# Kernel optimization log

Hardware: AMD Instinct MI355X
Metric: run time of the kernel (lower is better)

Reference implementation:

```python
import jax, jax.numpy as jnp
import numpy as np

B, S, DM = 1, 2048, 1024
H, D, T = 16, 64, 16
NA = 3  # anchor tiles per query (local tile appended -> 4 tiles, 64 tokens)


def setup_inputs() -> dict:
    key = jax.random.key(0)
    ks = jax.random.split(key, 6)
    sc = 1.0 / np.sqrt(DM)
    x = jax.random.normal(ks[0], (B, S, DM), jnp.float32)
    Wq = jax.random.normal(ks[1], (DM, H * D), jnp.float32) * sc
    Wk = jax.random.normal(ks[2], (DM, H * D), jnp.float32) * sc
    Wv = jax.random.normal(ks[3], (DM, H * D), jnp.float32) * sc
    Wo = jax.random.normal(ks[4], (H * D, DM), jnp.float32) * sc
    anchor_indices = jax.random.randint(ks[5], (B, H, S, NA), 0, S // T).astype(jnp.int32)
    # RoPE freqs: freqs_cis[s, j] = exp(i * s * theta_j), half-split convention
    half = D // 2
    inv_freq = 1.0 / (10000.0 ** (np.arange(half, dtype=np.float64) / half))
    ang = np.outer(np.arange(S), inv_freq)  # [S, half]
    cos = jnp.asarray(np.cos(ang), jnp.float32)
    sin = jnp.asarray(np.sin(ang), jnp.float32)
    return {"x": x, "Wq": Wq, "Wk": Wk, "Wv": Wv, "Wo": Wo,
            "cos": cos, "sin": sin, "anchor_indices": anchor_indices}


def _rotate_half(z):
    h = z.shape[-1] // 2
    return jnp.concatenate([-z[..., h:], z[..., :h]], axis=-1)


def reference(x, Wq, Wk, Wv, Wo, cos, sin, anchor_indices):
    b, s, _ = x.shape
    # projections -> [B, H, S, D]
    q = (x @ Wq).reshape(b, s, H, D).transpose(0, 2, 1, 3)
    k = (x @ Wk).reshape(b, s, H, D).transpose(0, 2, 1, 3)
    v = (x @ Wv).reshape(b, s, H, D).transpose(0, 2, 1, 3)
    # RoPE (half-split / rotate_half)
    cos_f = jnp.concatenate([cos, cos], axis=-1)[None, None]  # [1,1,S,D]
    sin_f = jnp.concatenate([sin, sin], axis=-1)[None, None]
    q = q * cos_f + _rotate_half(q) * sin_f
    k = k * cos_f + _rotate_half(k) * sin_f
    # tile index set: anchor tiles + local tile
    local = (jnp.arange(s) // T).astype(jnp.int32)
    local = jnp.broadcast_to(local[None, None, :, None], (b, H, s, 1))
    tiles = jnp.concatenate([anchor_indices, local], axis=-1)  # [B,H,S,NA+1]
    tok = tiles[..., None] * T + jnp.arange(T, dtype=jnp.int32)  # [B,H,S,NA+1,T]
    K = (NA + 1) * T  # sparse_len
    idx = jnp.clip(tok.reshape(b, H, s, K), 0, s - 1)
    # per-(b,h) per-query gather of K/V -> [B,H,S,K,D]
    gather = jax.vmap(jax.vmap(lambda kv, i: kv[i]))
    k_sp = gather(k, idx)
    v_sp = gather(v, idx)
    logits = jnp.einsum('bhqd,bhqkd->bhqk', q, k_sp) / jnp.sqrt(jnp.float32(D))
    qidx = jnp.arange(s)[None, None, :, None]
    fut = idx > qidx  # causal mask over gathered keys
    logits = jnp.where(fut, -1e10, logits)
    w = jax.nn.softmax(logits, axis=-1)
    fully_masked = jnp.all(fut, axis=-1, keepdims=True)
    w = jnp.where(fully_masked, 0.0, w)
    w = jnp.where(jnp.isnan(w), 0.0, w)
    out = jnp.einsum('bhqk,bhqkd->bhqd', w, v_sp)
    out = out.transpose(0, 2, 1, 3).reshape(b, s, H * D)
    return out @ Wo
```

## Files before the change

### kernel.cpp

```cpp
#include <hip/hip_runtime.h>
#include <hip/hip_bf16.h>


#define S_LEN 2048
#define DM 1024
#define NH 16
#define HD 64

typedef __bf16 bf16x8 __attribute__((ext_vector_type(8)));
typedef float f32x4 __attribute__((ext_vector_type(4)));

static __device__ __forceinline__ unsigned short f2bf(float f) {
    union { float f; unsigned int i; } un;
    un.f = f;
    unsigned int r = un.i + 0x7FFFu + ((un.i >> 16) & 1u);
    return (unsigned short)(r >> 16);
}
static __device__ __forceinline__ float bfu2f(unsigned short u) {
    union { unsigned int i; float f; } un;
    un.i = ((unsigned int)u) << 16;
    return un.f;
}
static __device__ __forceinline__ float bflo(unsigned int u) {
    union { unsigned int i; float f; } un;
    un.i = u << 16;
    return un.f;
}
static __device__ __forceinline__ float bfhi(unsigned int u) {
    union { unsigned int i; float f; } un;
    un.i = u & 0xFFFF0000u;
    return un.f;
}

static __device__ __forceinline__ void gll16(const unsigned short* g,
                                             unsigned short* l) {
    __builtin_amdgcn_global_load_lds(
        (const __attribute__((address_space(1))) unsigned int*)(uintptr_t)g,
        (__attribute__((address_space(3))) unsigned int*)(uintptr_t)l,
        16, 0, 0);
}

__global__ __launch_bounds__(256) void prep(
    const float* __restrict__ x, unsigned short* __restrict__ xb,
    const float* __restrict__ W0, const float* __restrict__ W1,
    const float* __restrict__ W2, const float* __restrict__ W3,
    unsigned short* __restrict__ T0, unsigned short* __restrict__ T1,
    unsigned short* __restrict__ T2, unsigned short* __restrict__ T3) {
    const int bx = blockIdx.x;
    if (bx < 4096) {
        const int z = bx >> 10, rem = bx & 1023;
        const float* W = (z == 0) ? W0 : (z == 1) ? W1 : (z == 2) ? W2 : W3;
        unsigned short* T = (z == 0) ? T0 : (z == 1) ? T1 : (z == 2) ? T2 : T3;
        __shared__ float t[32][33];
        const int bn = (rem & 31) * 32, bk = (rem >> 5) * 32;
        const int tx = threadIdx.x & 31, ty = threadIdx.x >> 5;
        #pragma unroll
        for (int m = 0; m < 4; ++m)
            t[ty + m * 8][tx] = W[(size_t)(bk + ty + m * 8) * 1024 + bn + tx];
        __syncthreads();
        #pragma unroll
        for (int m = 0; m < 4; ++m)
            T[(size_t)(bn + ty + m * 8) * 1024 + bk + tx] = f2bf(t[tx][ty + m * 8]);
    } else {
        const int i = (bx - 4096) * 2048 + threadIdx.x * 8;
        float4 f0 = *(const float4*)(x + i);
        float4 f1 = *(const float4*)(x + i + 4);
        ushort4 o0, o1;
        o0.x = f2bf(f0.x); o0.y = f2bf(f0.y); o0.z = f2bf(f0.z); o0.w = f2bf(f0.w);
        o1.x = f2bf(f1.x); o1.y = f2bf(f1.y); o1.z = f2bf(f1.z); o1.w = f2bf(f1.w);
        *(ushort4*)(xb + i) = o0;
        *(ushort4*)(xb + i + 4) = o1;
    }
}

__global__ __launch_bounds__(256) void gemm_qkv(
    const unsigned short* __restrict__ xb,
    const unsigned short* __restrict__ Wtq, const unsigned short* __restrict__ Wtk,
    const unsigned short* __restrict__ Wtv,
    unsigned short* __restrict__ qh, unsigned short* __restrict__ kh,
    unsigned short* __restrict__ vh,
    const float* __restrict__ cs, const float* __restrict__ sn) {
    __shared__ __align__(16) unsigned short Al[64 * 32];
    __shared__ __align__(16) unsigned short Bl[128 * 32];
    const int tid = threadIdx.x;
    const int nb = blockIdx.x >> 3;
    const unsigned short* __restrict__ Bt = (nb == 0) ? Wtq : (nb == 1) ? Wtk : Wtv;
    unsigned short* __restrict__ OUT = (nb == 0) ? qh : (nb == 1) ? kh : vh;
    const int col0 = (blockIdx.x & 7) * 128;
    const int row0 = blockIdx.y * 64;
    const int lane = tid & 63, wvi = tid >> 6;
    const int wr = (wvi >> 1) * 32, wc = (wvi & 1) * 64;
    const int l15 = lane & 15, quad = lane >> 4;

    const int grow = lane >> 2;
    const int gkc = (lane & 3) * 8;
    const unsigned short* gA = xb + (size_t)(row0 + wvi * 16 + grow) * 1024 + gkc;
    const unsigned short* gB = Bt + (size_t)(col0 + wvi * 32 + grow) * 1024 + gkc;
    unsigned short* lA = Al + (wvi * 16) * 32;
    unsigned short* lB = Bl + (wvi * 32) * 32;

    f32x4 acc[2][4] = {};
    for (int k0 = 0; k0 < 1024; k0 += 32) {
        __syncthreads();
        gll16(gA + k0, lA);
        gll16(gB + k0, lB);
        gll16(gB + 16 * 1024 + k0, lB + 16 * 32);
        __syncthreads();
        bf16x8 af[2], bfr[4];
        #pragma unroll
        for (int i = 0; i < 2; ++i)
            af[i] = *(const bf16x8*)&Al[(wr + i * 16 + l15) * 32 + quad * 8];
        #pragma unroll
        for (int j = 0; j < 4; ++j)
            bfr[j] = *(const bf16x8*)&Bl[(wc + j * 16 + l15) * 32 + quad * 8];
        #pragma unroll
        for (int i = 0; i < 2; ++i)
            #pragma unroll
            for (int j = 0; j < 4; ++j)
                acc[i][j] = __builtin_amdgcn_mfma_f32_16x16x32_bf16(
                    af[i], bfr[j], acc[i][j], 0, 0, 0);
    }

    const int hh = ((blockIdx.x & 7) << 1) + (wc >> 6);
    const bool dorope = (nb != 2);
    #pragma unroll
    for (int i = 0; i < 2; ++i) {
        const int rowb = row0 + wr + i * 16 + quad * 4;
        #pragma unroll
        for (int r = 0; r < 4; ++r) {
            const int s = rowb + r;
            float v0 = acc[i][0][r], v1 = acc[i][1][r];
            float v2 = acc[i][2][r], v3 = acc[i][3][r];
            if (dorope) {
                float c0 = cs[s * 32 + l15],      s0 = sn[s * 32 + l15];
                float c1 = cs[s * 32 + 16 + l15], s1 = sn[s * 32 + 16 + l15];
                float lo0 = v0 * c0 - v2 * s0;
                float hi0 = v2 * c0 + v0 * s0;
                float lo1 = v1 * c1 - v3 * s1;
                float hi1 = v3 * c1 + v1 * s1;
                v0 = lo0; v1 = lo1; v2 = hi0; v3 = hi1;
            }
            unsigned short* op = OUT + (size_t)hh * (S_LEN * 64) + (size_t)s * 64 + l15;
            op[0]  = f2bf(v0);
            op[16] = f2bf(v1);
            op[32] = f2bf(v2);
            op[48] = f2bf(v3);
        }
    }
}

__global__ __launch_bounds__(256) void attn_kernel(
    const unsigned short* __restrict__ qh, const unsigned short* __restrict__ kh,
    const unsigned short* __restrict__ vh, const int* __restrict__ anc,
    unsigned short* __restrict__ att) {
    __shared__ __align__(16) float qs[4][64];
    __shared__ __align__(16) int   ts[4][64];
    __shared__ __align__(16) float ws[4][64];
    const int w4 = threadIdx.x >> 6;
    const int lane = threadIdx.x & 63;
    const int wid = (blockIdx.x << 2) + w4;
    const int h = wid >> 11;
    const int qi = wid & 2047;
    const size_t hb = (size_t)h * (S_LEN * 64);

    const float q_own = bfu2f(qh[hb + (size_t)qi * 64 + lane]);
    const int slot = lane >> 4;
    const int tile = (slot < 3) ? anc[((size_t)h * S_LEN + qi) * 3 + slot]
                                : (qi >> 4);
    const int tok_own = tile * 16 + (lane & 15);
    qs[w4][lane] = q_own;
    ts[w4][lane] = tok_own;

    const int c = lane & 3;
    const int t = lane >> 2;
    float qv[16];
    #pragma unroll
    for (int r = 0; r < 4; ++r) {
        float4 f = *(const float4*)&qs[w4][c * 16 + r * 4];
        qv[r * 4 + 0] = f.x; qv[r * 4 + 1] = f.y;
        qv[r * 4 + 2] = f.z; qv[r * 4 + 3] = f.w;
    }

    #pragma unroll
    for (int p = 0; p < 4; ++p) {
        const int tk = ts[w4][p * 16 + t];
        const unsigned short* kp = kh + hb + (size_t)tk * 64 + c * 16;
        const uint4 k0 = *(const uint4*)kp;
        const uint4 k1 = *(const uint4*)(kp + 8);
        float part;
        part = bflo(k0.x) * qv[0];
        part = fmaf(bfhi(k0.x), qv[1], part);
        part = fmaf(bflo(k0.y), qv[2], part);
        part = fmaf(bfhi(k0.y), qv[3], part);
        part = fmaf(bflo(k0.z), qv[4], part);
        part = fmaf(bfhi(k0.z), qv[5], part);
        part = fmaf(bflo(k0.w), qv[6], part);
        part = fmaf(bfhi(k0.w), qv[7], part);
        part = fmaf(bflo(k1.x), qv[8], part);
        part = fmaf(bfhi(k1.x), qv[9], part);
        part = fmaf(bflo(k1.y), qv[10], part);
        part = fmaf(bfhi(k1.y), qv[11], part);
        part = fmaf(bflo(k1.z), qv[12], part);
        part = fmaf(bfhi(k1.z), qv[13], part);
        part = fmaf(bflo(k1.w), qv[14], part);
        part = fmaf(bfhi(k1.w), qv[15], part);
        part += __shfl_xor(part, 1, 64);
        part += __shfl_xor(part, 2, 64);
        if (c == 0) ws[w4][p * 16 + t] = part;
    }

    float logit = ws[w4][lane];
    const bool fut = tok_own > qi;
    logit = fut ? -1e30f : logit * 0.125f;

    float m = logit;
    #pragma unroll
    for (int off = 32; off >= 1; off >>= 1)
        m = fmaxf(m, __shfl_xor(m, off, 64));
    const float e = fut ? 0.f : __expf(logit - m);
    float ssum = e;
    #pragma unroll
    for (int off = 32; off >= 1; off >>= 1)
        ssum += __shfl_xor(ssum, off, 64);
    ws[w4][lane] = e / ssum;

    const int tq = lane >> 4;
    const int dd = lane & 15;
    const unsigned short* vbase = vh + hb + dd * 4;
    float a0 = 0.f, a1 = 0.f, a2 = 0.f, a3 = 0.f;
    #pragma unroll
    for (int r = 0; r < 16; ++r) {
        const int kk = r * 4 + tq;
        const int tok = ts[w4][kk];
        const uint2 vv = *(const uint2*)(vbase + (size_t)tok * 64);
        const float w = ws[w4][kk];
        a0 = fmaf(w, bflo(vv.x), a0);
        a1 = fmaf(w, bfhi(vv.x), a1);
        a2 = fmaf(w, bflo(vv.y), a2);
        a3 = fmaf(w, bfhi(vv.y), a3);
    }
    a0 += __shfl_xor(a0, 16, 64); a0 += __shfl_xor(a0, 32, 64);
    a1 += __shfl_xor(a1, 16, 64); a1 += __shfl_xor(a1, 32, 64);
    a2 += __shfl_xor(a2, 16, 64); a2 += __shfl_xor(a2, 32, 64);
    a3 += __shfl_xor(a3, 16, 64); a3 += __shfl_xor(a3, 32, 64);
    if (tq == 0) {
        ushort4 o;
        o.x = f2bf(a0); o.y = f2bf(a1); o.z = f2bf(a2); o.w = f2bf(a3);
        *(ushort4*)&att[(size_t)qi * DM + h * HD + dd * 4] = o;
    }
}

__global__ __launch_bounds__(256) void gemm_out(
    const unsigned short* __restrict__ A, const unsigned short* __restrict__ Bt,
    float* __restrict__ C) {
    __shared__ __align__(16) unsigned short Al[64 * 32];
    __shared__ __align__(16) unsigned short Bl[64 * 32];
    const int tid = threadIdx.x;
    const int col0 = blockIdx.x * 64;
    const int row0 = blockIdx.y * 64;
    const int lane = tid & 63, wvi = tid >> 6;
    const int wr = (wvi >> 1) * 32, wc = (wvi & 1) * 32;
    const int l15 = lane & 15, quad = lane >> 4;

    const int grow = lane >> 2;
    const int gkc = (lane & 3) * 8;
    const unsigned short* gA = A + (size_t)(row0 + wvi * 16 + grow) * 1024 + gkc;
    const unsigned short* gB = Bt + (size_t)(col0 + wvi * 16 + grow) * 1024 + gkc;
    unsigned short* lA = Al + (wvi * 16) * 32;
    unsigned short* lB = Bl + (wvi * 16) * 32;

    f32x4 acc[2][2] = {};
    for (int k0 = 0; k0 < 1024; k0 += 32) {
        __syncthreads();
        gll16(gA + k0, lA);
        gll16(gB + k0, lB);
        __syncthreads();
        bf16x8 af[2], bfr[2];
        #pragma unroll
        for (int i = 0; i < 2; ++i)
            af[i] = *(const bf16x8*)&Al[(wr + i * 16 + l15) * 32 + quad * 8];
        #pragma unroll
        for (int j = 0; j < 2; ++j)
            bfr[j] = *(const bf16x8*)&Bl[(wc + j * 16 + l15) * 32 + quad * 8];
        #pragma unroll
        for (int i = 0; i < 2; ++i)
            #pragma unroll
            for (int j = 0; j < 2; ++j)
                acc[i][j] = __builtin_amdgcn_mfma_f32_16x16x32_bf16(
                    af[i], bfr[j], acc[i][j], 0, 0, 0);
    }
    #pragma unroll
    for (int i = 0; i < 2; ++i) {
        const int rowb = row0 + wr + i * 16 + quad * 4;
        #pragma unroll
        for (int r = 0; r < 4; ++r) {
            float* crow = C + (size_t)(rowb + r) * 1024 + col0 + wc;
            #pragma unroll
            for (int j = 0; j < 2; ++j)
                crow[j * 16 + l15] = acc[i][j][r];
        }
    }
}

extern "C" void kernel_launch(void* const* d_in, const int* in_sizes, int n_in,
                              void* d_out, int out_size, void* d_ws, size_t ws_size,
                              hipStream_t stream) {
    const float* x   = (const float*)d_in[0];
    const float* Wq  = (const float*)d_in[1];
    const float* Wk  = (const float*)d_in[2];
    const float* Wv  = (const float*)d_in[3];
    const float* Wo  = (const float*)d_in[4];
    const float* cs  = (const float*)d_in[5];
    const float* sn  = (const float*)d_in[6];
    const int*   anc = (const int*)d_in[7];
    float* out = (float*)d_out;

    unsigned short* xb  = (unsigned short*)d_ws;
    unsigned short* Wtq = xb  + (size_t)2048 * 1024;
    unsigned short* Wtk = Wtq + (size_t)1024 * 1024;
    unsigned short* Wtv = Wtk + (size_t)1024 * 1024;
    unsigned short* Wto = Wtv + (size_t)1024 * 1024;
    unsigned short* qh  = Wto + (size_t)1024 * 1024;
    unsigned short* kh  = qh  + (size_t)2048 * 1024;
    unsigned short* vh  = kh  + (size_t)2048 * 1024;
    unsigned short* att = vh  + (size_t)2048 * 1024;

    prep<<<5120, 256, 0, stream>>>(x, xb, Wq, Wk, Wv, Wo, Wtq, Wtk, Wtv, Wto);
    gemm_qkv<<<dim3(24, 32), 256, 0, stream>>>(xb, Wtq, Wtk, Wtv,
                                               qh, kh, vh, cs, sn);
    attn_kernel<<<(S_LEN * NH) / 4, 256, 0, stream>>>(qh, kh, vh, anc, att);
    gemm_out<<<dim3(16, 32), 256, 0, stream>>>(att, Wto, out);
}
```

Baseline: 151.9 us.

## Remove LDS staging in sparse attention and use DPP quad reductions

The attention kernel no longer stages q and token indices through shared memory. Each lane loads its q slice and the three anchor tile ids directly and computes token indices in registers. Cross-lane reductions within quads switch from ds_bpermute shuffles to DPP quad_perm, and the PV phase is remapped so that the 4 lanes of a quad split the keys, which lets that final reduction run entirely in DPP. The softmax weights are written to LDS transposed so each lane reads them as four vector loads. This cuts LDS traffic and shuffle latency, at the cost of redundant global reads of the anchor ids and less coalesced V access per wave.

```diff
diff --git a/kernel.cpp b/kernel.cpp
--- a/kernel.cpp
+++ b/kernel.cpp
@@ -30,6 +30,12 @@
     union { unsigned int i; float f; } un;
     un.i = u & 0xFFFF0000u;
     return un.f;
+}
+
+template <int CTRL>
+static __device__ __forceinline__ float qperm(float x) {
+    return __int_as_float(__builtin_amdgcn_update_dpp(
+        0, __float_as_int(x), CTRL, 0xF, 0xF, true));
 }
 
 static __device__ __forceinline__ void gll16(const unsigned short* g,
@@ -153,9 +159,8 @@
     const unsigned short* __restrict__ qh, const unsigned short* __restrict__ kh,
     const unsigned short* __restrict__ vh, const int* __restrict__ anc,
     unsigned short* __restrict__ att) {
-    __shared__ __align__(16) float qs[4][64];
-    __shared__ __align__(16) int   ts[4][64];
     __shared__ __align__(16) float ws[4][64];
+    __shared__ __align__(16) float ww[4][64];
     const int w4 = threadIdx.x >> 6;
     const int lane = threadIdx.x & 63;
     const int wid = (blockIdx.x << 2) + w4;
@@ -163,27 +168,32 @@
     const int qi = wid & 2047;
     const size_t hb = (size_t)h * (S_LEN * 64);
 
-    const float q_own = bfu2f(qh[hb + (size_t)qi * 64 + lane]);
-    const int slot = lane >> 4;
-    const int tile = (slot < 3) ? anc[((size_t)h * S_LEN + qi) * 3 + slot]
-                                : (qi >> 4);
-    const int tok_own = tile * 16 + (lane & 15);
-    qs[w4][lane] = q_own;
-    ts[w4][lane] = tok_own;
+    const size_t ab = ((size_t)h * S_LEN + qi) * 3;
+    const int t0 = anc[ab];
+    const int t1 = anc[ab + 1];
+    const int t2 = anc[ab + 2];
+    const int t3 = qi >> 4;
 
     const int c = lane & 3;
     const int t = lane >> 2;
+
+    const unsigned short* qp = qh + hb + (size_t)qi * 64 + c * 16;
+    const uint4 q0 = *(const uint4*)qp;
+    const uint4 q1 = *(const uint4*)(qp + 8);
     float qv[16];
-    #pragma unroll
-    for (int r = 0; r < 4; ++r) {
-        float4 f = *(const float4*)&qs[w4][c * 16 + r * 4];
-        qv[r * 4 + 0] = f.x; qv[r * 4 + 1] = f.y;
-        qv[r * 4 + 2] = f.z; qv[r * 4 + 3] = f.w;
-    }
+    qv[0]  = bflo(q0.x); qv[1]  = bfhi(q0.x);
+    qv[2]  = bflo(q0.y); qv[3]  = bfhi(q0.y);
+    qv[4]  = bflo(q0.z); qv[5]  = bfhi(q0.z);
+    qv[6]  = bflo(q0.w); qv[7]  = bfhi(q0.w);
+    qv[8]  = bflo(q1.x); qv[9]  = bfhi(q1.x);
+    qv[10] = bflo(q1.y); qv[11] = bfhi(q1.y);
+    qv[12] = bflo(q1.z); qv[13] = bfhi(q1.z);
+    qv[14] = bflo(q1.w); qv[15] = bfhi(q1.w);
 
     #pragma unroll
     for (int p = 0; p < 4; ++p) {
-        const int tk = ts[w4][p * 16 + t];
+        const int tile = (p == 0) ? t0 : (p == 1) ? t1 : (p == 2) ? t2 : t3;
+        const int tk = tile * 16 + t;
         const unsigned short* kp = kh + hb + (size_t)tk * 64 + c * 16;
         const uint4 k0 = *(const uint4*)kp;
         const uint4 k1 = *(const uint4*)(kp + 8);
@@ -204,45 +214,59 @@
         part = fmaf(bfhi(k1.z), qv[13], part);
         part = fmaf(bflo(k1.w), qv[14], part);
         part = fmaf(bfhi(k1.w), qv[15], part);
-        part += __shfl_xor(part, 1, 64);
-        part += __shfl_xor(part, 2, 64);
+        part += qperm<0xB1>(part);
+        part += qperm<0x4E>(part);
         if (c == 0) ws[w4][p * 16 + t] = part;
     }
 
     float logit = ws[w4][lane];
+    const int slot = lane >> 4;
+    const int tile_own = (slot == 0) ? t0 : (slot == 1) ? t1
+                       : (slot == 2) ? t2 : t3;
+    const int tok_own = tile_own * 16 + (lane & 15);
     const bool fut = tok_own > qi;
     logit = fut ? -1e30f : logit * 0.125f;
 
     float m = logit;
-    #pragma unroll
-    for (int off = 32; off >= 1; off >>= 1)
-        m = fmaxf(m, __shfl_xor(m, off, 64));
+    m = fmaxf(m, __shfl_xor(m, 32, 64));
+    m = fmaxf(m, __shfl_xor(m, 16, 64));
+    m = fmaxf(m, __shfl_xor(m, 8, 64));
+    m = fmaxf(m, __shfl_xor(m, 4, 64));
+    m = fmaxf(m, qperm<0x4E>(m));
+    m = fmaxf(m, qperm<0xB1>(m));
     const float e = fut ? 0.f : __expf(logit - m);
     float ssum = e;
-    #pragma unroll
-    for (int off = 32; off >= 1; off >>= 1)
-        ssum += __shfl_xor(ssum, off, 64);
-    ws[w4][lane] = e / ssum;
-
-    const int tq = lane >> 4;
-    const int dd = lane & 15;
+    ssum += __shfl_xor(ssum, 32, 64);
+    ssum += __shfl_xor(ssum, 16, 64);
+    ssum += __shfl_xor(ssum, 8, 64);
+    ssum += __shfl_xor(ssum, 4, 64);
+    ssum += qperm<0x4E>(ssum);
+    ssum += qperm<0xB1>(ssum);
+    ww[w4][(lane & 3) * 16 + (lane >> 2)] = e / ssum;
+
+    const int tq = lane & 3;
+    const int dd = lane >> 2;
     const unsigned short* vbase = vh + hb + dd * 4;
+    f32x4 wv[4];
+    #pragma unroll
+    for (int r4 = 0; r4 < 4; ++r4)
+        wv[r4] = *(const f32x4*)&ww[w4][tq * 16 + r4 * 4];
     float a0 = 0.f, a1 = 0.f, a2 = 0.f, a3 = 0.f;
     #pragma unroll
     for (int r = 0; r < 16; ++r) {
-        const int kk = r * 4 + tq;
-        const int tok = ts[w4][kk];
+        const int tile = (r < 4) ? t0 : (r < 8) ? t1 : (r < 12) ? t2 : t3;
+        const int tok = tile * 16 + (r & 3) * 4 + tq;
         const uint2 vv = *(const uint2*)(vbase + (size_t)tok * 64);
-        const float w = ws[w4][kk];
+        const float w = wv[r >> 2][r & 3];
         a0 = fmaf(w, bflo(vv.x), a0);
         a1 = fmaf(w, bfhi(vv.x), a1);
         a2 = fmaf(w, bflo(vv.y), a2);
         a3 = fmaf(w, bfhi(vv.y), a3);
     }
-    a0 += __shfl_xor(a0, 16, 64); a0 += __shfl_xor(a0, 32, 64);
-    a1 += __shfl_xor(a1, 16, 64); a1 += __shfl_xor(a1, 32, 64);
-    a2 += __shfl_xor(a2, 16, 64); a2 += __shfl_xor(a2, 32, 64);
-    a3 += __shfl_xor(a3, 16, 64); a3 += __shfl_xor(a3, 32, 64);
+    a0 += qperm<0xB1>(a0); a0 += qperm<0x4E>(a0);
+    a1 += qperm<0xB1>(a1); a1 += qperm<0x4E>(a1);
+    a2 += qperm<0xB1>(a2); a2 += qperm<0x4E>(a2);
+    a3 += qperm<0xB1>(a3); a3 += qperm<0x4E>(a3);
     if (tq == 0) {
         ushort4 o;
         o.x = f2bf(a0); o.y = f2bf(a1); o.z = f2bf(a2); o.w = f2bf(a3);
```

Measured after the change: 193.1 us. 1.27x slower.
